# Optimization experiments

Hardware: AMD Instinct MI355X
Metric: run time of the kernel (lower is better)

The kernel has to match this reference:

```python
import jax, jax.numpy as jnp
import numpy as np

N_NODES = 100000
N_EDGES = 1600000
IN_F = 512
OUT_F = 128


def setup_inputs() -> dict:
    key = jax.random.key(0)
    k1, k2, k3, k4, k5 = jax.random.split(key, 5)
    x = jax.random.normal(k1, (N_NODES, IN_F), dtype=jnp.float32)
    adj_row = jnp.sort(jax.random.randint(k2, (N_EDGES,), 0, N_NODES, dtype=jnp.int32))
    adj_col = jax.random.randint(k3, (N_EDGES,), 0, N_NODES, dtype=jnp.int32)
    adj_vals = jax.random.uniform(k4, (N_EDGES,), dtype=jnp.float32)
    # Xavier-uniform init like nn.init.xavier_uniform_
    limit = float(np.sqrt(6.0 / (IN_F + OUT_F)))
    weight = jax.random.uniform(k5, (IN_F, OUT_F), minval=-limit, maxval=limit, dtype=jnp.float32)
    return {"x": x, "adj_row": adj_row, "adj_col": adj_col, "adj_vals": adj_vals, "weight": weight}


def reference(x, adj_row, adj_col, adj_vals, weight):
    # support = input @ weight  (dense GEMM; torch.spmm with dense-equivalent input)
    support = x @ weight                      # [N, OUT_F]
    # output = adj @ support, adj in COO: gather cols, scale, segment-sum by row
    msgs = adj_vals[:, None] * support[adj_col]          # [E, OUT_F]
    output = jax.ops.segment_sum(msgs, adj_row, num_segments=N_NODES)  # [N, OUT_F]
    return output
```

## Files before the change

kernel.cpp:

```cpp
#include <hip/hip_runtime.h>
#include <hip/hip_bf16.h>

typedef __bf16 bf16;
typedef __attribute__((ext_vector_type(8))) __bf16 bf16x8;
typedef __attribute__((ext_vector_type(4))) __bf16 bf16x4;
typedef __attribute__((ext_vector_type(2))) __bf16 bf16x2;
typedef __attribute__((ext_vector_type(4))) float f32x4;

#define IN_F 512
#define OUT_F 128
#define BM 64
#define BK 64
#define NKT (IN_F / BK)
#define RPW 8
#define WPB 4
#define PAGE 256
#define UNR 16
#define WT_BLOCKS 256

__global__ __launch_bounds__(256) void setup_kernel(const float* __restrict__ w,
                                                    bf16* __restrict__ wt_frag,
                                                    const int* __restrict__ adj_row,
                                                    int* __restrict__ row_ptr,
                                                    int n_edges, int n_nodes) {
    if (blockIdx.x < WT_BLOCKS) {
        int o = blockIdx.x * 256 + threadIdx.x;
        int e   = o & 7;
        int l   = (o >> 3) & 63;
        int nb  = (o >> 9) & 7;
        int kkt = o >> 12;
        int n = nb * 16 + (l & 15);
        int k = (kkt >> 1) * 64 + (kkt & 1) * 32 + (l >> 4) * 8 + e;
        wt_frag[o] = (bf16)w[k * OUT_F + n];
    } else {
        int e = (blockIdx.x - WT_BLOCKS) * 256 + threadIdx.x;
        if (e >= n_edges) return;
        int r1 = adj_row[e];
        int r0 = (e == 0) ? -1 : adj_row[e - 1];
        for (int r = r0 + 1; r <= r1; ++r) row_ptr[r] = e;
        if (e == n_edges - 1)
            for (int r = r1 + 1; r <= n_nodes; ++r) row_ptr[r] = n_edges;
    }
}

__global__ __launch_bounds__(256) void gemm_kernel(const float* __restrict__ x,
                                                   const bf16* __restrict__ wt_frag,
                                                   bf16* __restrict__ support,
                                                   int n_nodes) {
    __shared__ bf16 As[2][BM * BK];

    const int tid  = threadIdx.x;
    const int lane = tid & 63;
    const int wid  = tid >> 6;
    const int row0 = blockIdx.x * BM;

    float4 av[3][4];
    bf16x8 bfr[2][2][2];

    auto load_tile = [&](int set, int kt) {
        const int k0 = kt * BK;
        #pragma unroll
        for (int i = 0; i < 4; ++i) {
            int li = i * 256 + tid;
            int r = li >> 4, c4 = li & 15;
            int grow = row0 + r;
            float4 v = {0.f, 0.f, 0.f, 0.f};
            if (grow < n_nodes)
                v = *reinterpret_cast<const float4*>(x + (size_t)grow * IN_F + k0 + c4 * 4);
            av[set][i] = v;
        }
    };

    auto load_b = [&](int p, int kt) {
        #pragma unroll
        for (int kk = 0; kk < 2; ++kk)
            #pragma unroll
            for (int n = 0; n < 2; ++n) {
                int f = (kt * 2 + kk) * 8 + (wid * 2 + n);
                bfr[p][kk][n] = *reinterpret_cast<const bf16x8*>(wt_frag + ((size_t)f * 64 + lane) * 8);
            }
    };

    auto write_tile = [&](int set, int buf) {
        char* Ab = (char*)As[buf];
        #pragma unroll
        for (int i = 0; i < 4; ++i) {
            int li = i * 256 + tid;
            int r = li >> 4, c4 = li & 15;
            bf16x4 b;
            b[0] = (bf16)av[set][i].x; b[1] = (bf16)av[set][i].y;
            b[2] = (bf16)av[set][i].z; b[3] = (bf16)av[set][i].w;
            *reinterpret_cast<bf16x4*>(Ab + ((r * 128 + c4 * 8) ^ ((r & 7) << 4))) = b;
        }
    };

    load_tile(0, 0);
    write_tile(0, 0);
    load_tile(1, 1);
    load_tile(2, 2);
    load_b(0, 0);
    __syncthreads();

    f32x4 acc[4][2] = {};

    #pragma unroll
    for (int kt = 0; kt < NKT; ++kt) {
        if (kt + 1 < NKT) load_b((kt + 1) & 1, kt + 1);
        if (kt + 3 < NKT) load_tile(kt % 3, kt + 3);

        const char* Ab = (const char*)As[kt & 1];
        #pragma unroll
        for (int kk = 0; kk < 2; ++kk) {
            const int kbyte = kk * 64 + (lane >> 4) * 16;
            bf16x8 a[4];
            #pragma unroll
            for (int m = 0; m < 4; ++m) {
                int r = m * 16 + (lane & 15);
                a[m] = *reinterpret_cast<const bf16x8*>(Ab + ((r * 128 + kbyte) ^ ((r & 7) << 4)));
            }
            #pragma unroll
            for (int m = 0; m < 4; ++m)
                #pragma unroll
                for (int n = 0; n < 2; ++n)
                    acc[m][n] = __builtin_amdgcn_mfma_f32_16x16x32_bf16(a[m], bfr[kt & 1][kk][n], acc[m][n], 0, 0, 0);
        }

        if (kt + 1 < NKT) {
            write_tile((kt + 1) % 3, (kt + 1) & 1);
            __syncthreads();
        }
    }

    #pragma unroll
    for (int m = 0; m < 4; ++m) {
        #pragma unroll
        for (int n = 0; n < 2; ++n) {
            #pragma unroll
            for (int j = 0; j < 4; ++j) {
                int gm = row0 + m * 16 + (lane >> 4) * 4 + j;
                int gn = wid * 32 + n * 16 + (lane & 15);
                if (gm < n_nodes)
                    support[(size_t)gm * OUT_F + gn] = (bf16)acc[m][n][j];
            }
        }
    }
}

__global__ __launch_bounds__(256, 8) void scatter_kernel(const int* __restrict__ adj_row,
                                                         const int* __restrict__ adj_col,
                                                         const float* __restrict__ adj_vals,
                                                         const bf16* __restrict__ support,
                                                         const int* __restrict__ row_ptr,
                                                         float* __restrict__ out,
                                                         int n_nodes) {
    __shared__ int   srow[WPB][PAGE];
    __shared__ int   scol[WPB][PAGE];
    __shared__ float sval[WPB][PAGE];

    const int t  = threadIdx.x & 63;
    const int w  = threadIdx.x >> 6;
    const int r0 = blockIdx.x * (WPB * RPW) + w * RPW;
    if (r0 >= n_nodes) return;
    const int rEnd = min(r0 + RPW, n_nodes);
    const int eLo  = row_ptr[r0];
    const int eHi  = row_ptr[rEnd];

    float accx = 0.f, accy = 0.f;
    int   cur  = r0;

    auto flush_to = [&](int rNew) {
        if (cur < rEnd) {
            float2 st = {accx, accy};
            *reinterpret_cast<float2*>(out + (size_t)cur * OUT_F + t * 2) = st;
        }
        float2 z = {0.f, 0.f};
        int zhi = rNew < rEnd ? rNew : rEnd;
        for (int r = cur + 1; r < zhi; ++r)
            *reinterpret_cast<float2*>(out + (size_t)r * OUT_F + t * 2) = z;
        accx = 0.f; accy = 0.f;
        cur = rNew;
    };

    for (int base = eLo; base < eHi; base += PAGE) {
        const int nE = min(PAGE, eHi - base);
        for (int i = t; i < nE; i += 64) {
            srow[w][i] = adj_row[base + i];
            scol[w][i] = adj_col[base + i];
            sval[w][i] = adj_vals[base + i];
        }
        const int nEpad = (nE + UNR - 1) & ~(UNR - 1);
        {
            int i = nE + t;
            if (i < nEpad) {
                srow[w][i] = n_nodes;
                scol[w][i] = 0;
                sval[w][i] = 0.f;
            }
        }

        for (int i0 = 0; i0 < nE; i0 += UNR) {
            unsigned int u[UNR];
            #pragma unroll
            for (int k = 0; k < UNR; ++k) {
                int c = scol[w][i0 + k];
                u[k] = *reinterpret_cast<const unsigned int*>(support + (size_t)c * OUT_F + t * 2);
            }
            #pragma unroll
            for (int k = 0; k < UNR; ++k) {
                int r = srow[w][i0 + k];
                if (r != cur) flush_to(r);
                float  s = sval[w][i0 + k];
                bf16x2 v = __builtin_bit_cast(bf16x2, u[k]);
                accx += s * (float)v[0];
                accy += s * (float)v[1];
            }
        }
    }
    flush_to(rEnd);
}

extern "C" void kernel_launch(void* const* d_in, const int* in_sizes, int n_in,
                              void* d_out, int out_size, void* d_ws, size_t ws_size,
                              hipStream_t stream) {
    const float* x        = (const float*)d_in[0];
    const int*   adj_row  = (const int*)d_in[1];
    const int*   adj_col  = (const int*)d_in[2];
    const float* adj_vals = (const float*)d_in[3];
    const float* weight   = (const float*)d_in[4];
    float*       out      = (float*)d_out;

    const int n_nodes = in_sizes[0] / IN_F;
    const int n_edges = in_sizes[1];

    char* ws = (char*)d_ws;
    bf16* support = (bf16*)ws;
    bf16* wt_frag = (bf16*)(ws + (size_t)n_nodes * OUT_F * 2);
    int*  row_ptr = (int*)(ws + (size_t)n_nodes * OUT_F * 2 + IN_F * OUT_F * 2);

    int setup_blocks = WT_BLOCKS + (n_edges + 255) / 256;
    setup_kernel<<<setup_blocks, 256, 0, stream>>>(weight, wt_frag, adj_row,
                                                   row_ptr, n_edges, n_nodes);

    int gemm_blocks = (n_nodes + BM - 1) / BM;
    gemm_kernel<<<gemm_blocks, 256, 0, stream>>>(x, wt_frag, support, n_nodes);

    int scat_blocks = (n_nodes + WPB * RPW - 1) / (WPB * RPW);
    scatter_kernel<<<scat_blocks, WPB * 64, 0, stream>>>(adj_row, adj_col, adj_vals,
                                                         support, row_ptr, out, n_nodes);
}
```

Before: 122.4 us.

## Load GEMM A fragments directly from global into registers using 32x32 MFMA

The GEMM no longer stages the fp32 input tile through shared memory. Each wave loads its 32 rows straight from global memory into registers in MFMA fragment order, converts them to bf16 in registers, and issues 32x32x16 bf16 MFMAs across all 128 output columns. The weight fragment layout is reshaped to match. This removes the LDS writes, the swizzled reads and the barriers, at the cost of less coalesced strided global reads of x, more B-fragment registers per wave, and a larger tile of 128 rows per block.

```diff
diff --git a/kernel.cpp b/kernel.cpp
--- a/kernel.cpp
+++ b/kernel.cpp
@@ -3,15 +3,14 @@
 
 typedef __bf16 bf16;
 typedef __attribute__((ext_vector_type(8))) __bf16 bf16x8;
-typedef __attribute__((ext_vector_type(4))) __bf16 bf16x4;
 typedef __attribute__((ext_vector_type(2))) __bf16 bf16x2;
 typedef __attribute__((ext_vector_type(4))) float f32x4;
+typedef __attribute__((ext_vector_type(16))) float f32x16;
 
 #define IN_F 512
 #define OUT_F 128
-#define BM 64
-#define BK 64
-#define NKT (IN_F / BK)
+#define BM 128
+#define NKT 8
 #define RPW 8
 #define WPB 4
 #define PAGE 256
@@ -27,10 +26,10 @@
         int o = blockIdx.x * 256 + threadIdx.x;
         int e   = o & 7;
         int l   = (o >> 3) & 63;
-        int nb  = (o >> 9) & 7;
-        int kkt = o >> 12;
-        int n = nb * 16 + (l & 15);
-        int k = (kkt >> 1) * 64 + (kkt & 1) * 32 + (l >> 4) * 8 + e;
+        int nb2 = (o >> 9) & 3;
+        int kkt = o >> 11;
+        int n = nb2 * 32 + (l & 31);
+        int k = (kkt >> 2) * 64 + (kkt & 3) * 16 + (l >> 5) * 8 + e;
         wt_frag[o] = (bf16)w[k * OUT_F + n];
     } else {
         int e = (blockIdx.x - WT_BLOCKS) * 256 + threadIdx.x;
@@ -47,101 +46,64 @@
                                                    const bf16* __restrict__ wt_frag,
                                                    bf16* __restrict__ support,
                                                    int n_nodes) {
-    __shared__ bf16 As[2][BM * BK];
-
-    const int tid  = threadIdx.x;
-    const int lane = tid & 63;
-    const int wid  = tid >> 6;
-    const int row0 = blockIdx.x * BM;
-
-    float4 av[3][4];
-    bf16x8 bfr[2][2][2];
-
-    auto load_tile = [&](int set, int kt) {
-        const int k0 = kt * BK;
-        #pragma unroll
-        for (int i = 0; i < 4; ++i) {
-            int li = i * 256 + tid;
-            int r = li >> 4, c4 = li & 15;
-            int grow = row0 + r;
-            float4 v = {0.f, 0.f, 0.f, 0.f};
-            if (grow < n_nodes)
-                v = *reinterpret_cast<const float4*>(x + (size_t)grow * IN_F + k0 + c4 * 4);
-            av[set][i] = v;
+    const int tid   = threadIdx.x;
+    const int lane  = tid & 63;
+    const int wrow0 = blockIdx.x * BM + (tid >> 6) * 32;
+    const int grow  = min(wrow0 + (lane & 31), n_nodes - 1);
+    const float* xr = x + (size_t)grow * IN_F + (lane >> 5) * 8;
+
+    f32x4 av[2][8];
+    auto load_a = [&](int set, int kt) {
+        #pragma unroll
+        for (int j = 0; j < 4; ++j) {
+            av[set][j * 2]     = *reinterpret_cast<const f32x4*>(xr + kt * 64 + j * 16);
+            av[set][j * 2 + 1] = *reinterpret_cast<const f32x4*>(xr + kt * 64 + j * 16 + 4);
         }
     };
 
-    auto load_b = [&](int p, int kt) {
-        #pragma unroll
-        for (int kk = 0; kk < 2; ++kk)
-            #pragma unroll
-            for (int n = 0; n < 2; ++n) {
-                int f = (kt * 2 + kk) * 8 + (wid * 2 + n);
-                bfr[p][kk][n] = *reinterpret_cast<const bf16x8*>(wt_frag + ((size_t)f * 64 + lane) * 8);
-            }
+    bf16x8 bfr[4][4];
+    auto load_b = [&](int kt) {
+        #pragma unroll
+        for (int j = 0; j < 4; ++j)
+            #pragma unroll
+            for (int nb = 0; nb < 4; ++nb)
+                bfr[j][nb] = *reinterpret_cast<const bf16x8*>(
+                    wt_frag + ((size_t)(kt * 16 + j * 4 + nb) * 64 + lane) * 8);
     };
 
-    auto write_tile = [&](int set, int buf) {
-        char* Ab = (char*)As[buf];
-        #pragma unroll
-        for (int i = 0; i < 4; ++i) {
-            int li = i * 256 + tid;
-            int r = li >> 4, c4 = li & 15;
-            bf16x4 b;
-            b[0] = (bf16)av[set][i].x; b[1] = (bf16)av[set][i].y;
-            b[2] = (bf16)av[set][i].z; b[3] = (bf16)av[set][i].w;
-            *reinterpret_cast<bf16x4*>(Ab + ((r * 128 + c4 * 8) ^ ((r & 7) << 4))) = b;
-        }
-    };
-
-    load_tile(0, 0);
-    write_tile(0, 0);
-    load_tile(1, 1);
-    load_tile(2, 2);
-    load_b(0, 0);
-    __syncthreads();
-
-    f32x4 acc[4][2] = {};
+    load_b(0);
+    load_a(0, 0);
+    load_a(1, 1);
+
+    f32x16 acc[4] = {};
 
     #pragma unroll
     for (int kt = 0; kt < NKT; ++kt) {
-        if (kt + 1 < NKT) load_b((kt + 1) & 1, kt + 1);
-        if (kt + 3 < NKT) load_tile(kt % 3, kt + 3);
-
-        const char* Ab = (const char*)As[kt & 1];
-        #pragma unroll
-        for (int kk = 0; kk < 2; ++kk) {
-            const int kbyte = kk * 64 + (lane >> 4) * 16;
-            bf16x8 a[4];
-            #pragma unroll
-            for (int m = 0; m < 4; ++m) {
-                int r = m * 16 + (lane & 15);
-                a[m] = *reinterpret_cast<const bf16x8*>(Ab + ((r * 128 + kbyte) ^ ((r & 7) << 4)));
-            }
-            #pragma unroll
-            for (int m = 0; m < 4; ++m)
-                #pragma unroll
-                for (int n = 0; n < 2; ++n)
-                    acc[m][n] = __builtin_amdgcn_mfma_f32_16x16x32_bf16(a[m], bfr[kt & 1][kk][n], acc[m][n], 0, 0, 0);
-        }
-
-        if (kt + 1 < NKT) {
-            write_tile((kt + 1) % 3, (kt + 1) & 1);
-            __syncthreads();
-        }
+        bf16x8 afr[4];
+        #pragma unroll
+        for (int j = 0; j < 4; ++j) {
+            f32x4 lo = av[kt & 1][j * 2], hi = av[kt & 1][j * 2 + 1];
+            afr[j][0] = (bf16)lo[0]; afr[j][1] = (bf16)lo[1];
+            afr[j][2] = (bf16)lo[2]; afr[j][3] = (bf16)lo[3];
+            afr[j][4] = (bf16)hi[0]; afr[j][5] = (bf16)hi[1];
+            afr[j][6] = (bf16)hi[2]; afr[j][7] = (bf16)hi[3];
+        }
+        #pragma unroll
+        for (int j = 0; j < 4; ++j)
+            #pragma unroll
+            for (int nb = 0; nb < 4; ++nb)
+                acc[nb] = __builtin_amdgcn_mfma_f32_32x32x16_bf16(afr[j], bfr[j][nb], acc[nb], 0, 0, 0);
+        if (kt + 1 < NKT) load_b(kt + 1);
+        if (kt + 2 < NKT) load_a(kt & 1, kt + 2);
     }
 
     #pragma unroll
-    for (int m = 0; m < 4; ++m) {
-        #pragma unroll
-        for (int n = 0; n < 2; ++n) {
-            #pragma unroll
-            for (int j = 0; j < 4; ++j) {
-                int gm = row0 + m * 16 + (lane >> 4) * 4 + j;
-                int gn = wid * 32 + n * 16 + (lane & 15);
-                if (gm < n_nodes)
-                    support[(size_t)gm * OUT_F + gn] = (bf16)acc[m][n][j];
-            }
+    for (int nb = 0; nb < 4; ++nb) {
+        #pragma unroll
+        for (int rg = 0; rg < 16; ++rg) {
+            int gm = wrow0 + (rg & 3) + 8 * (rg >> 2) + 4 * (lane >> 5);
+            if (gm < n_nodes)
+                support[(size_t)gm * OUT_F + nb * 32 + (lane & 31)] = (bf16)acc[nb][rg];
         }
     }
 }
```

Result: slower. 148.2 us (+21.1%).
